# Optimization experiments

Hardware: AMD Instinct MI355X
Metric: run time of the kernel (lower is better)

Reference implementation:

```python
import jax, jax.numpy as jnp
import numpy as np

NUM_LEVELS = 8
CODEBOOK_SIZE = 1024
EMBED_DIM = 256
BETA = 0.25
N_TOKENS = 65536
EPS = 1e-6


def setup_inputs() -> dict:
    key = jax.random.key(0)
    kz, kc = jax.random.split(key)
    z = jax.random.normal(kz, (N_TOKENS, EMBED_DIM), dtype=jnp.float32)
    # per-level init std = 1 / 2**i, matching nn.init.normal_ in __init__
    scales = (0.5 ** jnp.arange(NUM_LEVELS, dtype=jnp.float32))[:, None, None]
    codebooks = jax.random.normal(kc, (NUM_LEVELS, CODEBOOK_SIZE, EMBED_DIM), dtype=jnp.float32) * scales
    return {"z": z, "codebooks": codebooks}


def _normalize(v):
    # F.normalize(p=2, dim=-1, eps=1e-6): v / max(||v||, eps)
    return v / jnp.maximum(jnp.linalg.norm(v, axis=-1, keepdims=True), EPS)


def _rotation_trick(x, quantized):
    sg = jax.lax.stop_gradient
    u = _normalize(x)
    q = _normalize(quantized)
    w = _normalize(u + q)
    xw_dot = jnp.sum(x * sg(w), axis=-1, keepdims=True)
    xu_dot = jnp.sum(x * sg(u), axis=-1, keepdims=True)
    return x - 2.0 * xw_dot * sg(w) + 2.0 * xu_dot * sg(q)


def reference(z, codebooks):
    sg = jax.lax.stop_gradient
    residual = z
    quantized_sum = jnp.zeros_like(z)
    indices_list = []
    total_codebook_loss = jnp.float32(0.0)
    total_commitment_loss = jnp.float32(0.0)
    for lvl in range(NUM_LEVELS):
        c = codebooks[lvl]  # [K, D]
        # squared-euclidean distances up to constant ||x||^2 (argmin-equivalent, as in source)
        c_sq = jnp.sum(c * c, axis=1)                      # [K]
        dists = c_sq - 2.0 * (residual @ c.T)              # [N, K]
        min_idx = jnp.argmin(dists, axis=-1)               # [N]
        indices_list.append(min_idx)
        z_q_local = c[min_idx]                             # gather [N, D]
        total_codebook_loss = total_codebook_loss + jnp.mean((z_q_local - sg(residual)) ** 2)
        total_commitment_loss = total_commitment_loss + jnp.mean((sg(z_q_local) - residual) ** 2)
        # training path uses the rotation-trick estimator
        z_q_st = _rotation_trick(residual, z_q_local)
        residual = residual - z_q_st
        quantized_sum = quantized_sum + z_q_local
    indices = jnp.stack(indices_list, axis=-1)             # [N, L]
    loss = total_codebook_loss + BETA * total_commitment_loss
    # perplexity (codebook utilization entropy)
    flat = indices.reshape(-1)
    counts = jnp.zeros((CODEBOOK_SIZE,), jnp.float32).at[flat].add(1.0)
    probs = counts / jnp.float32(flat.size)
    safe = jnp.where(probs > 0, probs, 1.0)
    entropy = -jnp.sum(probs * jnp.log(safe))
    perplexity = jnp.exp(entropy)
    # straight-through output
    z_q = z + sg(quantized_sum - z)
    return (z_q, indices, loss, total_codebook_loss, total_commitment_loss, perplexity)
```

## Files before the change

### kernel.cpp

```cpp
#include <hip/hip_runtime.h>

#define N_TOK 65536
#define DIM 256
#define KCB 1024
#define NLVL 8
#define TPB 32
#define ND_OUT (N_TOK * DIM)
#define IDX_OFF ND_OUT
#define SC_OFF (ND_OUT + N_TOK * NLVL)
#define EPSV 1e-6f

typedef _Float16 half8 __attribute__((ext_vector_type(8)));
typedef float f32x4 __attribute__((ext_vector_type(4)));

__device__ __forceinline__ float wave_red(float v) {
    v += __shfl_xor(v, 32, 64);
    v += __shfl_xor(v, 16, 64);
    v += __shfl_xor(v, 8, 64);
    v += __shfl_xor(v, 4, 64);
    v += __shfl_xor(v, 2, 64);
    v += __shfl_xor(v, 1, 64);
    return v;
}

__device__ __forceinline__ unsigned int ordf(float d) {
    unsigned int u = __float_as_uint(d);
    return (u & 0x80000000u) ? ~u : (u ^ 0x80000000u);
}

__global__ __launch_bounds__(256) void k_prep(const float* __restrict__ cbs,
                                              half8* __restrict__ ws_b) {
    const int lvl = blockIdx.x >> 6, ntg = blockIdx.x & 63;
    const int lane = threadIdx.x & 63, sg = threadIdx.x >> 6;
    const float sc = (float)(1 << (lvl + 5));
#pragma unroll
    for (int ss = 0; ss < 2; ++ss) {
        const int s = sg + ss * 4;
        const int code = ntg * 16 + (lane & 15);
        const int d0 = s * 32 + (lane >> 4) * 8;
        const float* p = cbs + ((size_t)(lvl * KCB + code)) * DIM + d0;
        const float4 va = *(const float4*)p;
        const float4 vb = *(const float4*)(p + 4);
        float f[8] = {va.x, va.y, va.z, va.w, vb.x, vb.y, vb.z, vb.w};
        half8 h, l;
#pragma unroll
        for (int j = 0; j < 8; ++j) {
            float fs = f[j] * sc;
            _Float16 hh = (_Float16)fs;
            h[j] = hh;
            l[j] = (_Float16)(fs - (float)hh);
        }
        const size_t base = ((size_t)((lvl * 8 + s) * 64 + ntg)) * 128;
        ws_b[base + lane] = h;
        ws_b[base + 64 + lane] = l;
    }
}

__global__ __launch_bounds__(256) void k_csq(const float* __restrict__ cbs,
                                             float* __restrict__ csq_s,
                                             int* __restrict__ gcounts,
                                             float* __restrict__ gloss) {
    const int tid = threadIdx.x;
    const int wv = tid >> 6, lane = tid & 63;
    const int code = blockIdx.x * 4 + wv;
    const float4 v = *(const float4*)(cbs + (size_t)code * DIM + lane * 4);
    float s = v.x * v.x + v.y * v.y + v.z * v.z + v.w * v.w;
    s = wave_red(s);
    const int lvl = code >> 10;
    if (lane == 0) csq_s[code] = s * (float)(1 << (10 + lvl));
    if (blockIdx.x == 0) {
#pragma unroll
        for (int i = 0; i < 4; ++i) gcounts[tid + i * 256] = 0;
        if (tid == 0) *gloss = 0.f;
    }
}

__global__ __launch_bounds__(256, 4) void k_main(const float* __restrict__ z,
                                                 const float* __restrict__ cbs,
                                                 const half8* __restrict__ ws_b,
                                                 const float* __restrict__ csq_s,
                                                 float* __restrict__ out,
                                                 int* __restrict__ gcounts,
                                                 float* __restrict__ gloss) {
    __shared__ __align__(16) float Rld[TPB * DIM];
    __shared__ unsigned long long keyBuf[4][TPB];
    __shared__ int bestI_sh[TPB];
    __shared__ int idxBuf[TPB * NLVL];
    __shared__ int hist[KCB];
    __shared__ float wpart[4];

    const int tid = threadIdx.x;
    const int lane = tid & 63, q = tid >> 6;
    const int l15 = lane & 15, qd = lane >> 4;
    const int t0 = blockIdx.x * TPB;

#pragma unroll
    for (int i = 0; i < 8; ++i) {
        int fi = tid + i * 256;
        int t = fi >> 6, k4 = fi & 63;
        float4 v = *(const float4*)(z + (size_t)(t0 + t) * DIM + k4 * 4);
        v.x *= 32.f; v.y *= 32.f; v.z *= 32.f; v.w *= 32.f;
        *(float4*)&Rld[t * DIM + ((k4 ^ (t & 15)) << 2)] = v;
    }
#pragma unroll
    for (int i = 0; i < 4; ++i) hist[tid + i * 256] = 0;
    float loss_acc = 0.f;
    __syncthreads();

    for (int lvl = 0; lvl < NLVL; ++lvl) {
        float bd[8];
        int bi[8];
#pragma unroll
        for (int i = 0; i < 8; ++i) { bd[i] = 3.402823466e38f; bi[i] = 0; }

        for (int hf = 0; hf < 2; ++hf) {
            f32x4 acc[8][2];
#pragma unroll
            for (int nt = 0; nt < 8; ++nt)
#pragma unroll
                for (int m = 0; m < 2; ++m) acc[nt][m] = (f32x4){0.f, 0.f, 0.f, 0.f};

#pragma unroll 1
            for (int s = 0; s < 8; ++s) {
                half8 Ah[2], Al[2];
#pragma unroll
                for (int m = 0; m < 2; ++m) {
                    const int row = (m * 16 + l15) * DIM;
                    const int k4 = 8 * s + 2 * qd;
                    float4 va = *(const float4*)&Rld[row + ((k4 ^ l15) << 2)];
                    float4 vb = *(const float4*)&Rld[row + (((k4 + 1) ^ l15) << 2)];
                    float f[8] = {va.x, va.y, va.z, va.w, vb.x, vb.y, vb.z, vb.w};
                    half8 h, l;
#pragma unroll
                    for (int j = 0; j < 8; ++j) {
                        _Float16 hh = (_Float16)f[j];
                        h[j] = hh;
                        l[j] = (_Float16)(f[j] - (float)hh);
                    }
                    Ah[m] = h;
                    Al[m] = l;
                }
                const half8* pb = ws_b +
                    (((size_t)(lvl * 8 + s)) * 64 + q * 16 + hf * 8) * 128 + lane;
                half8 bh = pb[0], bl = pb[64];
#pragma unroll
                for (int nt = 0; nt < 8; ++nt) {
                    const int off = (nt < 7) ? (nt + 1) * 128 : (s < 7 ? 64 * 128 : 0);
                    half8 nbh = pb[off];
                    half8 nbl = pb[off + 64];
                    acc[nt][0] = __builtin_amdgcn_mfma_f32_16x16x32_f16(Ah[0], bh, acc[nt][0], 0, 0, 0);
                    acc[nt][1] = __builtin_amdgcn_mfma_f32_16x16x32_f16(Ah[1], bh, acc[nt][1], 0, 0, 0);
                    acc[nt][0] = __builtin_amdgcn_mfma_f32_16x16x32_f16(Al[0], bh, acc[nt][0], 0, 0, 0);
                    acc[nt][1] = __builtin_amdgcn_mfma_f32_16x16x32_f16(Al[1], bh, acc[nt][1], 0, 0, 0);
                    acc[nt][0] = __builtin_amdgcn_mfma_f32_16x16x32_f16(Ah[0], bl, acc[nt][0], 0, 0, 0);
                    acc[nt][1] = __builtin_amdgcn_mfma_f32_16x16x32_f16(Ah[1], bl, acc[nt][1], 0, 0, 0);
                    acc[nt][0] = __builtin_amdgcn_mfma_f32_16x16x32_f16(Al[0], bl, acc[nt][0], 0, 0, 0);
                    acc[nt][1] = __builtin_amdgcn_mfma_f32_16x16x32_f16(Al[1], bl, acc[nt][1], 0, 0, 0);
                    bh = nbh;
                    bl = nbl;
                }
            }
            const float* csqp = csq_s + lvl * KCB + q * 256 + hf * 128 + l15;
#pragma unroll
            for (int nt = 0; nt < 8; ++nt) {
                const float cs = csqp[nt * 16];
                const int code = q * 256 + hf * 128 + nt * 16 + l15;
#pragma unroll
                for (int i = 0; i < 4; ++i) {
                    float d0 = fmaf(-2.f, acc[nt][0][i], cs);
                    if (d0 < bd[i]) { bd[i] = d0; bi[i] = code; }
                    float d1 = fmaf(-2.f, acc[nt][1][i], cs);
                    if (d1 < bd[4 + i]) { bd[4 + i] = d1; bi[4 + i] = code; }
                }
            }
        }
        unsigned long long key[8];
#pragma unroll
        for (int i = 0; i < 8; ++i)
            key[i] = (((unsigned long long)ordf(bd[i])) << 10) | (unsigned long long)bi[i];
#pragma unroll
        for (int m = 1; m <= 8; m <<= 1)
#pragma unroll
            for (int i = 0; i < 8; ++i) {
                unsigned long long o = __shfl_xor(key[i], m, 64);
                if (o < key[i]) key[i] = o;
            }
        if (l15 == 0) {
#pragma unroll
            for (int m = 0; m < 2; ++m)
#pragma unroll
                for (int i = 0; i < 4; ++i)
                    keyBuf[q][m * 16 + qd * 4 + i] = key[m * 4 + i];
        }
        __syncthreads();
        if (tid < TPB) {
            unsigned long long k = keyBuf[0][tid];
            if (keyBuf[1][tid] < k) k = keyBuf[1][tid];
            if (keyBuf[2][tid] < k) k = keyBuf[2][tid];
            if (keyBuf[3][tid] < k) k = keyBuf[3][tid];
            const int idx = (int)(k & 1023ull);
            bestI_sh[tid] = idx;
            idxBuf[tid * NLVL + lvl] = idx;
            atomicAdd(&hist[idx], 1);
        }
        __syncthreads();

        const float* cb = cbs + (size_t)lvl * KCB * DIM;
        for (int s2 = 0; s2 < 8; ++s2) {
            const int tl = q * 8 + s2;
            const int idx = bestI_sh[tl];
            const int e = tl & 15;
            float4 r4 = *(const float4*)&Rld[tl * DIM + ((lane ^ e) << 2)];
            r4.x *= 0.03125f; r4.y *= 0.03125f; r4.z *= 0.03125f; r4.w *= 0.03125f;
            float4 c4 = *(const float4*)(cb + (size_t)idx * DIM + lane * 4);
            float rr = r4.x * r4.x + r4.y * r4.y + r4.z * r4.z + r4.w * r4.w;
            float cc = c4.x * c4.x + c4.y * c4.y + c4.z * c4.z + c4.w * c4.w;
            float e0 = (c4.x - r4.x) * (c4.x - r4.x) + (c4.y - r4.y) * (c4.y - r4.y) +
                       (c4.z - r4.z) * (c4.z - r4.z) + (c4.w - r4.w) * (c4.w - r4.w);
            rr = wave_red(rr);
            cc = wave_red(cc);
            e0 = wave_red(e0);
            const float dx = fmaxf(sqrtf(rr), EPSV);
            const float dc = fmaxf(sqrtf(cc), EPSV);
            float4 u4 = make_float4(r4.x / dx, r4.y / dx, r4.z / dx, r4.w / dx);
            float4 q4 = make_float4(c4.x / dc, c4.y / dc, c4.z / dc, c4.w / dc);
            float4 w4 = make_float4(u4.x + q4.x, u4.y + q4.y, u4.z + q4.z, u4.w + q4.w);
            float ww = w4.x * w4.x + w4.y * w4.y + w4.z * w4.z + w4.w * w4.w;
            float xw = r4.x * w4.x + r4.y * w4.y + r4.z * w4.z + r4.w * w4.w;
            float xu = r4.x * u4.x + r4.y * u4.y + r4.z * u4.z + r4.w * u4.w;
            ww = wave_red(ww);
            xw = wave_red(xw);
            xu = wave_red(xu);
            const float dw = fmaxf(sqrtf(ww), EPSV);
            const float xwn = xw / dw;
            float4 wn = make_float4(w4.x / dw, w4.y / dw, w4.z / dw, w4.w / dw);
            float4 zst = make_float4(r4.x - 2.f * xwn * wn.x + 2.f * xu * q4.x,
                                     r4.y - 2.f * xwn * wn.y + 2.f * xu * q4.y,
                                     r4.z - 2.f * xwn * wn.z + 2.f * xu * q4.z,
                                     r4.w - 2.f * xwn * wn.w + 2.f * xu * q4.w);
            float4 rn = make_float4((r4.x - zst.x) * 32.f, (r4.y - zst.y) * 32.f,
                                    (r4.z - zst.z) * 32.f, (r4.w - zst.w) * 32.f);
            *(float4*)&Rld[tl * DIM + ((lane ^ e) << 2)] = rn;
            loss_acc += e0;
        }
        __syncthreads();
    }

    for (int s2 = 0; s2 < 8; ++s2) {
        const int tl = q * 8 + s2;
        const size_t trow = t0 + tl;
        float4 z4 = *(const float4*)(z + trow * DIM + lane * 4);
        float4 qs = make_float4(0.f, 0.f, 0.f, 0.f);
#pragma unroll
        for (int lvl = 0; lvl < NLVL; ++lvl) {
            const int idx = idxBuf[tl * NLVL + lvl];
            float4 c4 = *(const float4*)(cbs + ((size_t)(lvl * KCB + idx)) * DIM + lane * 4);
            qs.x += c4.x; qs.y += c4.y; qs.z += c4.z; qs.w += c4.w;
        }
        float4 o = make_float4(z4.x + (qs.x - z4.x), z4.y + (qs.y - z4.y),
                               z4.z + (qs.z - z4.z), z4.w + (qs.w - z4.w));
        *(float4*)(out + trow * DIM + lane * 4) = o;
    }
    out[IDX_OFF + (size_t)(t0 + (tid >> 3)) * NLVL + (tid & 7)] = (float)idxBuf[tid];
#pragma unroll
    for (int i = 0; i < 4; ++i) {
        int b = tid + i * 256;
        int h = hist[b];
        if (h) atomicAdd(&gcounts[b], h);
    }
    if (lane == 0) wpart[q] = loss_acc;
    __syncthreads();
    if (tid == 0) atomicAdd(gloss, wpart[0] + wpart[1] + wpart[2] + wpart[3]);
}

__global__ __launch_bounds__(256) void k_fin(const int* __restrict__ gcounts,
                                             const float* __restrict__ gloss,
                                             float* __restrict__ out) {
    __shared__ float part[4];
    const int tid = threadIdx.x, lane = tid & 63, wv = tid >> 6;
    float e = 0.f;
#pragma unroll
    for (int i = 0; i < 4; ++i) {
        float c = (float)gcounts[tid * 4 + i];
        float p = c * (1.f / 524288.f);
        if (p > 0.f) e += p * logf(p);
    }
    e = wave_red(e);
    if (lane == 0) part[wv] = e;
    __syncthreads();
    if (tid == 0) {
        float ent = -(part[0] + part[1] + part[2] + part[3]);
        float cbl = *gloss * (1.f / 16777216.f);
        out[SC_OFF + 0] = cbl + 0.25f * cbl;
        out[SC_OFF + 1] = cbl;
        out[SC_OFF + 2] = cbl;
        out[SC_OFF + 3] = expf(ent);
    }
}

extern "C" void kernel_launch(void* const* d_in, const int* in_sizes, int n_in,
                              void* d_out, int out_size, void* d_ws, size_t ws_size,
                              hipStream_t stream) {
    (void)in_sizes; (void)n_in; (void)out_size; (void)ws_size;
    const float* z = (const float*)d_in[0];
    const float* cbs = (const float*)d_in[1];
    float* out = (float*)d_out;
    half8* ws_b = (half8*)d_ws;
    float* csq = (float*)((char*)d_ws + (8u << 20));
    int* gcounts = (int*)((char*)d_ws + (8u << 20) + 32768);
    float* gloss = (float*)((char*)d_ws + (8u << 20) + 32768 + 4096);

    hipLaunchKernelGGL(k_prep, dim3(512), dim3(256), 0, stream, cbs, ws_b);
    hipLaunchKernelGGL(k_csq, dim3(2048), dim3(256), 0, stream, cbs, csq, gcounts, gloss);
    hipLaunchKernelGGL(k_main, dim3(2048), dim3(256), 0, stream, z, cbs, ws_b, csq, out,
                       gcounts, gloss);
    hipLaunchKernelGGL(k_fin, dim3(1), dim3(256), 0, stream, gcounts, gloss, out);
}
```

Before: 1.459 ms.

## Double token tile to 64 per block with 8 waves each owning 128 codes

The main kernel now processes 64 tokens per block with 512 threads. Each of 8 waves covers 128 codes in a single pass over four 16-row M tiles, instead of two passes over two tiles. Each loaded B fragment now feeds four MFMA rows, halving global codebook reads per token. The B prefetch also carries across s-steps and levels without a reload. In exchange the kernel needs roughly double the accumulator and argmin registers and more LDS per block, so occupancy may drop, and the per-level sync now spans 8 waves.

```diff
diff --git a/kernel.cpp b/kernel.cpp
--- a/kernel.cpp
+++ b/kernel.cpp
@@ -4,7 +4,7 @@
 #define DIM 256
 #define KCB 1024
 #define NLVL 8
-#define TPB 32
+#define TPB 64
 #define ND_OUT (N_TOK * DIM)
 #define IDX_OFF ND_OUT
 #define SC_OFF (ND_OUT + N_TOK * NLVL)
@@ -75,7 +75,7 @@
     }
 }
 
-__global__ __launch_bounds__(256, 4) void k_main(const float* __restrict__ z,
+__global__ __launch_bounds__(512, 2) void k_main(const float* __restrict__ z,
                                                  const float* __restrict__ cbs,
                                                  const half8* __restrict__ ws_b,
                                                  const float* __restrict__ csq_s,
@@ -83,121 +83,126 @@
                                                  int* __restrict__ gcounts,
                                                  float* __restrict__ gloss) {
     __shared__ __align__(16) float Rld[TPB * DIM];
-    __shared__ unsigned long long keyBuf[4][TPB];
+    __shared__ unsigned long long keyBuf[8][TPB];
     __shared__ int bestI_sh[TPB];
     __shared__ int idxBuf[TPB * NLVL];
     __shared__ int hist[KCB];
-    __shared__ float wpart[4];
+    __shared__ float wpart[8];
 
     const int tid = threadIdx.x;
-    const int lane = tid & 63, q = tid >> 6;
+    const int lane = tid & 63, w = tid >> 6;
     const int l15 = lane & 15, qd = lane >> 4;
     const int t0 = blockIdx.x * TPB;
 
 #pragma unroll
     for (int i = 0; i < 8; ++i) {
-        int fi = tid + i * 256;
+        int fi = tid + i * 512;
         int t = fi >> 6, k4 = fi & 63;
         float4 v = *(const float4*)(z + (size_t)(t0 + t) * DIM + k4 * 4);
         v.x *= 32.f; v.y *= 32.f; v.z *= 32.f; v.w *= 32.f;
         *(float4*)&Rld[t * DIM + ((k4 ^ (t & 15)) << 2)] = v;
     }
 #pragma unroll
-    for (int i = 0; i < 4; ++i) hist[tid + i * 256] = 0;
+    for (int i = 0; i < 2; ++i) hist[tid + i * 512] = 0;
     float loss_acc = 0.f;
+
+    const half8* pbw = ws_b + (size_t)(w * 8) * 128 + lane;
+    half8 bh = pbw[0], bl = pbw[64];
     __syncthreads();
 
     for (int lvl = 0; lvl < NLVL; ++lvl) {
-        float bd[8];
-        int bi[8];
-#pragma unroll
-        for (int i = 0; i < 8; ++i) { bd[i] = 3.402823466e38f; bi[i] = 0; }
-
-        for (int hf = 0; hf < 2; ++hf) {
-            f32x4 acc[8][2];
-#pragma unroll
-            for (int nt = 0; nt < 8; ++nt)
-#pragma unroll
-                for (int m = 0; m < 2; ++m) acc[nt][m] = (f32x4){0.f, 0.f, 0.f, 0.f};
+        float bd[16];
+        int bi[16];
+#pragma unroll
+        for (int i = 0; i < 16; ++i) { bd[i] = 3.402823466e38f; bi[i] = 0; }
+
+        f32x4 acc[8][4];
+#pragma unroll
+        for (int nt = 0; nt < 8; ++nt)
+#pragma unroll
+            for (int m = 0; m < 4; ++m) acc[nt][m] = (f32x4){0.f, 0.f, 0.f, 0.f};
 
 #pragma unroll 1
-            for (int s = 0; s < 8; ++s) {
-                half8 Ah[2], Al[2];
-#pragma unroll
-                for (int m = 0; m < 2; ++m) {
-                    const int row = (m * 16 + l15) * DIM;
-                    const int k4 = 8 * s + 2 * qd;
-                    float4 va = *(const float4*)&Rld[row + ((k4 ^ l15) << 2)];
-                    float4 vb = *(const float4*)&Rld[row + (((k4 + 1) ^ l15) << 2)];
-                    float f[8] = {va.x, va.y, va.z, va.w, vb.x, vb.y, vb.z, vb.w};
-                    half8 h, l;
-#pragma unroll
-                    for (int j = 0; j < 8; ++j) {
-                        _Float16 hh = (_Float16)f[j];
-                        h[j] = hh;
-                        l[j] = (_Float16)(f[j] - (float)hh);
-                    }
-                    Ah[m] = h;
-                    Al[m] = l;
+        for (int s = 0; s < 8; ++s) {
+            half8 Ah[4], Al[4];
+#pragma unroll
+            for (int m = 0; m < 4; ++m) {
+                const int row = (m * 16 + l15) * DIM;
+                const int k4 = 8 * s + 2 * qd;
+                float4 va = *(const float4*)&Rld[row + ((k4 ^ l15) << 2)];
+                float4 vb = *(const float4*)&Rld[row + (((k4 + 1) ^ l15) << 2)];
+                float f[8] = {va.x, va.y, va.z, va.w, vb.x, vb.y, vb.z, vb.w};
+                half8 h, l;
+#pragma unroll
+                for (int j = 0; j < 8; ++j) {
+                    _Float16 hh = (_Float16)f[j];
+                    h[j] = hh;
+                    l[j] = (_Float16)(f[j] - (float)hh);
                 }
-                const half8* pb = ws_b +
-                    (((size_t)(lvl * 8 + s)) * 64 + q * 16 + hf * 8) * 128 + lane;
-                half8 bh = pb[0], bl = pb[64];
-#pragma unroll
-                for (int nt = 0; nt < 8; ++nt) {
-                    const int off = (nt < 7) ? (nt + 1) * 128 : (s < 7 ? 64 * 128 : 0);
-                    half8 nbh = pb[off];
-                    half8 nbl = pb[off + 64];
-                    acc[nt][0] = __builtin_amdgcn_mfma_f32_16x16x32_f16(Ah[0], bh, acc[nt][0], 0, 0, 0);
-                    acc[nt][1] = __builtin_amdgcn_mfma_f32_16x16x32_f16(Ah[1], bh, acc[nt][1], 0, 0, 0);
-                    acc[nt][0] = __builtin_amdgcn_mfma_f32_16x16x32_f16(Al[0], bh, acc[nt][0], 0, 0, 0);
-                    acc[nt][1] = __builtin_amdgcn_mfma_f32_16x16x32_f16(Al[1], bh, acc[nt][1], 0, 0, 0);
-                    acc[nt][0] = __builtin_amdgcn_mfma_f32_16x16x32_f16(Ah[0], bl, acc[nt][0], 0, 0, 0);
-                    acc[nt][1] = __builtin_amdgcn_mfma_f32_16x16x32_f16(Ah[1], bl, acc[nt][1], 0, 0, 0);
-                    acc[nt][0] = __builtin_amdgcn_mfma_f32_16x16x32_f16(Al[0], bl, acc[nt][0], 0, 0, 0);
-                    acc[nt][1] = __builtin_amdgcn_mfma_f32_16x16x32_f16(Al[1], bl, acc[nt][1], 0, 0, 0);
-                    bh = nbh;
-                    bl = nbl;
-                }
+                Ah[m] = h;
+                Al[m] = l;
             }
-            const float* csqp = csq_s + lvl * KCB + q * 256 + hf * 128 + l15;
+            const half8* pb = ws_b + (((size_t)(lvl * 8 + s)) * 64 + w * 8) * 128 + lane;
+#pragma unroll
+            for (int nt = 0; nt < 8; ++nt) {
+                const int off = (nt < 7) ? (nt + 1) * 128 : 64 * 128;
+                half8 nbh = pb[off];
+                half8 nbl = pb[off + 64];
+#pragma unroll
+                for (int m = 0; m < 4; ++m)
+                    acc[nt][m] = __builtin_amdgcn_mfma_f32_16x16x32_f16(Ah[m], bh, acc[nt][m], 0, 0, 0);
+#pragma unroll
+                for (int m = 0; m < 4; ++m)
+                    acc[nt][m] = __builtin_amdgcn_mfma_f32_16x16x32_f16(Al[m], bh, acc[nt][m], 0, 0, 0);
+#pragma unroll
+                for (int m = 0; m < 4; ++m)
+                    acc[nt][m] = __builtin_amdgcn_mfma_f32_16x16x32_f16(Ah[m], bl, acc[nt][m], 0, 0, 0);
+#pragma unroll
+                for (int m = 0; m < 4; ++m)
+                    acc[nt][m] = __builtin_amdgcn_mfma_f32_16x16x32_f16(Al[m], bl, acc[nt][m], 0, 0, 0);
+                bh = nbh;
+                bl = nbl;
+            }
+        }
+        {
+            const float* csqp = csq_s + lvl * KCB + w * 128 + l15;
 #pragma unroll
             for (int nt = 0; nt < 8; ++nt) {
                 const float cs = csqp[nt * 16];
-                const int code = q * 256 + hf * 128 + nt * 16 + l15;
-#pragma unroll
-                for (int i = 0; i < 4; ++i) {
-                    float d0 = fmaf(-2.f, acc[nt][0][i], cs);
-                    if (d0 < bd[i]) { bd[i] = d0; bi[i] = code; }
-                    float d1 = fmaf(-2.f, acc[nt][1][i], cs);
-                    if (d1 < bd[4 + i]) { bd[4 + i] = d1; bi[4 + i] = code; }
-                }
+                const int code = w * 128 + nt * 16 + l15;
+#pragma unroll
+                for (int m = 0; m < 4; ++m)
+#pragma unroll
+                    for (int i = 0; i < 4; ++i) {
+                        float d = fmaf(-2.f, acc[nt][m][i], cs);
+                        if (d < bd[m * 4 + i]) { bd[m * 4 + i] = d; bi[m * 4 + i] = code; }
+                    }
             }
         }
-        unsigned long long key[8];
-#pragma unroll
-        for (int i = 0; i < 8; ++i)
+        unsigned long long key[16];
+#pragma unroll
+        for (int i = 0; i < 16; ++i)
             key[i] = (((unsigned long long)ordf(bd[i])) << 10) | (unsigned long long)bi[i];
 #pragma unroll
         for (int m = 1; m <= 8; m <<= 1)
 #pragma unroll
-            for (int i = 0; i < 8; ++i) {
+            for (int i = 0; i < 16; ++i) {
                 unsigned long long o = __shfl_xor(key[i], m, 64);
                 if (o < key[i]) key[i] = o;
             }
         if (l15 == 0) {
 #pragma unroll
-            for (int m = 0; m < 2; ++m)
+            for (int m = 0; m < 4; ++m)
 #pragma unroll
                 for (int i = 0; i < 4; ++i)
-                    keyBuf[q][m * 16 + qd * 4 + i] = key[m * 4 + i];
+                    keyBuf[w][m * 16 + qd * 4 + i] = key[m * 4 + i];
         }
         __syncthreads();
         if (tid < TPB) {
             unsigned long long k = keyBuf[0][tid];
-            if (keyBuf[1][tid] < k) k = keyBuf[1][tid];
-            if (keyBuf[2][tid] < k) k = keyBuf[2][tid];
-            if (keyBuf[3][tid] < k) k = keyBuf[3][tid];
+#pragma unroll
+            for (int ww = 1; ww < 8; ++ww)
+                if (keyBuf[ww][tid] < k) k = keyBuf[ww][tid];
             const int idx = (int)(k & 1023ull);
             bestI_sh[tid] = idx;
             idxBuf[tid * NLVL + lvl] = idx;
@@ -207,7 +212,7 @@
 
         const float* cb = cbs + (size_t)lvl * KCB * DIM;
         for (int s2 = 0; s2 < 8; ++s2) {
-            const int tl = q * 8 + s2;
+            const int tl = w * 8 + s2;
             const int idx = bestI_sh[tl];
             const int e = tl & 15;
             float4 r4 = *(const float4*)&Rld[tl * DIM + ((lane ^ e) << 2)];
@@ -247,7 +252,7 @@
     }
 
     for (int s2 = 0; s2 < 8; ++s2) {
-        const int tl = q * 8 + s2;
+        const int tl = w * 8 + s2;
         const size_t trow = t0 + tl;
         float4 z4 = *(const float4*)(z + trow * DIM + lane * 4);
         float4 qs = make_float4(0.f, 0.f, 0.f, 0.f);
@@ -263,14 +268,19 @@
     }
     out[IDX_OFF + (size_t)(t0 + (tid >> 3)) * NLVL + (tid & 7)] = (float)idxBuf[tid];
 #pragma unroll
-    for (int i = 0; i < 4; ++i) {
-        int b = tid + i * 256;
+    for (int i = 0; i < 2; ++i) {
+        int b = tid + i * 512;
         int h = hist[b];
         if (h) atomicAdd(&gcounts[b], h);
     }
-    if (lane == 0) wpart[q] = loss_acc;
+    if (lane == 0) wpart[w] = loss_acc;
     __syncthreads();
-    if (tid == 0) atomicAdd(gloss, wpart[0] + wpart[1] + wpart[2] + wpart[3]);
+    if (tid == 0) {
+        float sum = 0.f;
+#pragma unroll
+        for (int i = 0; i < 8; ++i) sum += wpart[i];
+        atomicAdd(gloss, sum);
+    }
 }
 
 __global__ __launch_bounds__(256) void k_fin(const int* __restrict__ gcounts,
@@ -312,7 +322,7 @@
 
     hipLaunchKernelGGL(k_prep, dim3(512), dim3(256), 0, stream, cbs, ws_b);
     hipLaunchKernelGGL(k_csq, dim3(2048), dim3(256), 0, stream, cbs, csq, gcounts, gloss);
-    hipLaunchKernelGGL(k_main, dim3(2048), dim3(256), 0, stream, z, cbs, ws_b, csq, out,
+    hipLaunchKernelGGL(k_main, dim3(1024), dim3(512), 0, stream, z, cbs, ws_b, csq, out,
                        gcounts, gloss);
     hipLaunchKernelGGL(k_fin, dim3(1), dim3(256), 0, stream, gcounts, gloss, out);
 }
```

Result: faster. 1.396 ms (-4.4%).
